# Kernel optimization log

Hardware: AMD Instinct MI355X
Metric: run time of the kernel (lower is better)

Reference implementation:

```python
import jax, jax.numpy as jnp
import numpy as np

N = 50000      # nodes
E = 1_600_000  # edges
IN, H, H2, OUT = 256, 128, 64, 2
EPS = 1e-5     # BatchNorm eps


def setup_inputs() -> dict:
    key = jax.random.key(0)
    ks = jax.random.split(key, 18)
    inp = {
        "x": jax.random.normal(ks[0], (N, IN), dtype=jnp.float32),
        "edge_index": jax.random.randint(ks[1], (2, E), 0, N, dtype=jnp.int64),
        # GCNConv 1
        "W1": jax.random.normal(ks[2], (IN, H), dtype=jnp.float32) / np.sqrt(IN),
        "b1": jnp.zeros((H,), dtype=jnp.float32),
        "g1": jnp.ones((H,), dtype=jnp.float32),
        "be1": jnp.zeros((H,), dtype=jnp.float32),
        "m1": jax.random.normal(ks[3], (H,), dtype=jnp.float32) * 0.1,
        "v1": jax.random.uniform(ks[4], (H,), dtype=jnp.float32, minval=0.5, maxval=1.5),
        # GCNConv 2
        "W2": jax.random.normal(ks[5], (H, H2), dtype=jnp.float32) / np.sqrt(H),
        "b2": jnp.zeros((H2,), dtype=jnp.float32),
        "g2": jnp.ones((H2,), dtype=jnp.float32),
        "be2": jnp.zeros((H2,), dtype=jnp.float32),
        "m2": jax.random.normal(ks[6], (H2,), dtype=jnp.float32) * 0.1,
        "v2": jax.random.uniform(ks[7], (H2,), dtype=jnp.float32, minval=0.5, maxval=1.5),
        # final linear
        "Wl": jax.random.normal(ks[8], (H2, OUT), dtype=jnp.float32) / np.sqrt(H2),
        "bl": jnp.zeros((OUT,), dtype=jnp.float32),
    }
    return inp


def _gcn_conv(x, W, b, src, dst, n_nodes):
    # PyG GCNConv: linear transform, then symmetric-normalized aggregation
    # with self-loops (gcn_norm, improved=False, fill_value=1).
    xw = x @ W                                            # [N, H]
    ones = jnp.ones((src.shape[0],), dtype=x.dtype)
    deg = jax.ops.segment_sum(ones, dst, num_segments=n_nodes) + 1.0  # +1 self-loop
    dinv = jax.lax.rsqrt(deg)                             # deg^{-1/2}
    norm = dinv[src] * dinv[dst]                          # [E]
    msgs = xw[src] * norm[:, None]                        # [E, H] gather
    agg = jax.ops.segment_sum(msgs, dst, num_segments=n_nodes)  # scatter-add
    agg = agg + xw * (1.0 / deg)[:, None]                 # self-loop term
    return agg + b


def _bn_relu(x, gamma, beta, mean, var):
    # inference-mode BatchNorm1d + ReLU
    xhat = (x - mean) * jax.lax.rsqrt(var + EPS)
    return jax.nn.relu(xhat * gamma + beta)


def reference(x, edge_index, W1, b1, g1, be1, m1, v1,
              W2, b2, g2, be2, m2, v2, Wl, bl):
    src, dst = edge_index[0], edge_index[1]
    h = _gcn_conv(x, W1, b1, src, dst, N)
    h = _bn_relu(h, g1, be1, m1, v1)
    # dropout is identity in eval mode
    h = _gcn_conv(h, W2, b2, src, dst, N)
    h = _bn_relu(h, g2, be2, m2, v2)
    return h @ Wl + bl
```

## Files before the change

kernel.cpp:

```cpp
#include <hip/hip_runtime.h>

#define N_NODES 50000
#define N_EDGES 1600000
#define IN_F 256
#define H1_F 128
#define H2_F 64
#define OUT_F 2
#define BN_EPS 1e-5f

#define NBUK 782
#define BCAP 3584
#define CHUNK 8192
#define NCHUNK 196

__device__ __forceinline__ unsigned short f2b(float f) {
    union { float f; unsigned u; } v; v.f = f;
    unsigned r = (v.u + 0x7FFFu + ((v.u >> 16) & 1u)) >> 16;
    return (unsigned short)r;
}
__device__ __forceinline__ float b2f(unsigned short b) {
    union { unsigned u; float f; } v; v.u = ((unsigned)b) << 16;
    return v.f;
}
__device__ __forceinline__ void add2(float& a0, float& a1, unsigned u) {
    union { unsigned u; float f; } lo, hi;
    lo.u = u << 16;
    hi.u = u & 0xFFFF0000u;
    a0 += lo.f; a1 += hi.f;
}

__launch_bounds__(512)
__global__ void chist_kernel(const int* __restrict__ dst, int* __restrict__ h) {
    __shared__ int lh[NBUK];
    const int c = blockIdx.x;
    for (int i = threadIdx.x; i < NBUK; i += 512) lh[i] = 0;
    __syncthreads();
    const int e0 = c * CHUNK;
    const int e1 = min(e0 + CHUNK, N_EDGES);
    for (int e = e0 + threadIdx.x; e < e1; e += 512)
        atomicAdd(&lh[dst[e] >> 6], 1);
    __syncthreads();
    for (int i = threadIdx.x; i < NBUK; i += 512)
        h[c * NBUK + i] = lh[i];
}

__global__ void bscan2_kernel(int* __restrict__ h, int* __restrict__ boff,
                              int* __restrict__ rowptr) {
    __shared__ int tmp[1024];
    const int t = threadIdx.x;
    int tot = 0;
    if (t < NBUK)
        for (int c = 0; c < NCHUNK; ++c) tot += h[c * NBUK + t];
    tmp[t] = tot;
    __syncthreads();
    for (int off = 1; off < 1024; off <<= 1) {
        int a = (t >= off) ? tmp[t - off] : 0;
        __syncthreads();
        tmp[t] += a;
        __syncthreads();
    }
    const int excl = tmp[t] - tot;
    if (t < NBUK) boff[t] = excl;
    if (t == 0) { boff[NBUK] = N_EDGES; rowptr[N_NODES] = N_EDGES; }
    if (t < NBUK) {
        int run = excl;
        for (int c = 0; c < NCHUNK; ++c) {
            int v = h[c * NBUK + t];
            h[c * NBUK + t] = run;
            run += v;
        }
    }
}

__launch_bounds__(512)
__global__ void cscatter_kernel(const int* __restrict__ src, const int* __restrict__ dst,
                                const int* __restrict__ h, unsigned* __restrict__ bedges) {
    __shared__ int cur[NBUK];
    const int c = blockIdx.x;
    for (int i = threadIdx.x; i < NBUK; i += 512) cur[i] = h[c * NBUK + i];
    __syncthreads();
    const int e0 = c * CHUNK;
    const int e1 = min(e0 + CHUNK, N_EDGES);
    for (int e = e0 + threadIdx.x; e < e1; e += 512) {
        int s = src[e];
        int d = dst[e];
        int slot = atomicAdd(&cur[d >> 6], 1);
        bedges[slot] = (unsigned)s | ((unsigned)d << 16);
    }
}

__launch_bounds__(256)
__global__ void build_kernel(const unsigned* __restrict__ bedges, const int* __restrict__ boff,
                             unsigned short* __restrict__ perm, int* __restrict__ rowptr,
                             float* __restrict__ dinv) {
    __shared__ unsigned e_lds[BCAP];
    __shared__ unsigned short p_lds[BCAP];
    __shared__ int ncnt[64], ncur[64];

    const int b = blockIdx.x;
    const int t = threadIdx.x;
    const int start = boff[b];
    const int end   = boff[b + 1];
    const int cnt   = end - start;
    const bool fits = (cnt <= BCAP);

    if (t < 64) ncnt[t] = 0;
    __syncthreads();

    for (int i = t; i < cnt; i += 256) {
        unsigned e = bedges[start + i];
        if (fits) e_lds[i] = e;
        atomicAdd(&ncnt[(e >> 16) & 63], 1);
    }
    __syncthreads();

    if (t == 0) {
        int a = 0;
        for (int i = 0; i < 64; ++i) { ncur[i] = a; a += ncnt[i]; }
    }
    __syncthreads();

    if (t < 64) {
        int node = b * 64 + t;
        if (node < N_NODES) {
            rowptr[node] = start + ncur[t];
            dinv[node]   = rsqrtf((float)ncnt[t] + 1.0f);
        }
    }
    __syncthreads();

    for (int i = t; i < cnt; i += 256) {
        unsigned e = fits ? e_lds[i] : bedges[start + i];
        int slot = atomicAdd(&ncur[(e >> 16) & 63], 1);
        unsigned short s = (unsigned short)(e & 0xFFFFu);
        if (fits) p_lds[slot] = s;
        else      perm[start + slot] = s;
    }
    if (fits) {
        __syncthreads();
        for (int i = t; i < cnt; i += 256) perm[start + i] = p_lds[i];
    }
}

template <typename AT, int BN, int TN>
__launch_bounds__(256)
__global__ void gemm_kernel(const AT* __restrict__ A, const float* __restrict__ B,
                            const float* __restrict__ dscale, unsigned short* __restrict__ C,
                            int M, int K) {
    constexpr int BM = 64;
    constexpr int BK = 16;
    __shared__ float As[BM][BK + 4];
    __shared__ float Bs[BK][BN];

    const int tid  = threadIdx.x;
    const int row0 = blockIdx.x * BM;
    const int tcol = tid & 15;
    const int trow = tid >> 4;

    float acc[4][TN];
#pragma unroll
    for (int i = 0; i < 4; ++i)
#pragma unroll
        for (int j = 0; j < TN; ++j) acc[i][j] = 0.f;

    const int arow = tid >> 2;
    const int acol = (tid & 3) << 2;
    int ar = row0 + arow;
    if (ar >= M) ar = M - 1;

    for (int k0 = 0; k0 < K; k0 += BK) {
        if constexpr (sizeof(AT) == 4) {
            float4 av = *(const float4*)((const float*)A + (size_t)ar * K + k0 + acol);
            *(float4*)(&As[arow][acol]) = av;
        } else {
            ushort4 av = *(const ushort4*)((const unsigned short*)A + (size_t)ar * K + k0 + acol);
            As[arow][acol + 0] = b2f(av.x);
            As[arow][acol + 1] = b2f(av.y);
            As[arow][acol + 2] = b2f(av.z);
            As[arow][acol + 3] = b2f(av.w);
        }
        constexpr int B4 = BN / 4;
#pragma unroll
        for (int l = tid; l < BK * B4; l += 256) {
            int brow = l / B4;
            int bcol = (l % B4) << 2;
            *(float4*)(&Bs[brow][bcol]) =
                *(const float4*)(B + (size_t)(k0 + brow) * BN + bcol);
        }
        __syncthreads();
#pragma unroll
        for (int kk = 0; kk < BK; ++kk) {
            float a[4];
#pragma unroll
            for (int i = 0; i < 4; ++i) a[i] = As[trow * 4 + i][kk];
            float b[TN];
#pragma unroll
            for (int j = 0; j < TN; ++j) b[j] = Bs[kk][tcol * TN + j];
#pragma unroll
            for (int i = 0; i < 4; ++i)
#pragma unroll
                for (int j = 0; j < TN; ++j) acc[i][j] += a[i] * b[j];
        }
        __syncthreads();
    }
#pragma unroll
    for (int i = 0; i < 4; ++i) {
        int r = row0 + trow * 4 + i;
        if (r < M) {
            float ds = dscale[r];
#pragma unroll
            for (int j = 0; j < TN; j += 4) {
                ushort4 o;
                o.x = f2b(acc[i][j + 0] * ds);
                o.y = f2b(acc[i][j + 1] * ds);
                o.z = f2b(acc[i][j + 2] * ds);
                o.w = f2b(acc[i][j + 3] * ds);
                *(ushort4*)(C + (size_t)r * BN + tcol * TN + j) = o;
            }
        }
    }
}

template <int HF, bool FINAL>
__launch_bounds__(256)
__global__ void agg_kernel(const int* __restrict__ rowptr, const unsigned short* __restrict__ perm,
                           const unsigned short* __restrict__ xwb, const float* __restrict__ dinv,
                           const float* __restrict__ bias, const float* __restrict__ g,
                           const float* __restrict__ be, const float* __restrict__ m,
                           const float* __restrict__ v, const float* __restrict__ Wl,
                           const float* __restrict__ bl, void* __restrict__ outp) {
    constexpr int FPQ = HF / 32;
    const int wid = (blockIdx.x * blockDim.x + threadIdx.x) >> 6;
    if (wid >= N_NODES) return;
    const int lane = threadIdx.x & 63;
    const int half = lane >> 5;
    const int l5   = lane & 31;
    const int f0   = l5 * FPQ;
    const int d    = wid;

    float acc[FPQ];
#pragma unroll
    for (int q = 0; q < FPQ; ++q) acc[q] = 0.f;

    if (half == 0) {
        if constexpr (FPQ == 4) {
            uint2 t = *(const uint2*)(xwb + (size_t)d * HF + f0);
            add2(acc[0], acc[1], t.x);
            add2(acc[2], acc[3], t.y);
        } else {
            unsigned t = *(const unsigned*)(xwb + (size_t)d * HF + f0);
            add2(acc[0], acc[1], t);
        }
    }

    const int start = rowptr[d];
    const int end   = rowptr[d + 1];
    for (int base = start; base < end; base += 64) {
        int pidx = base + lane;
        int pv = perm[pidx < end ? pidx : end - 1];
        int ne = end - base;
        if (ne > 64) ne = 64;
        if (ne == 64) {
#pragma unroll
            for (int j = 0; j < 64; j += 2) {
                int s = __shfl(pv, j + half);
                if constexpr (FPQ == 4) {
                    uint2 t = *(const uint2*)(xwb + (size_t)s * HF + f0);
                    add2(acc[0], acc[1], t.x);
                    add2(acc[2], acc[3], t.y);
                } else {
                    unsigned t = *(const unsigned*)(xwb + (size_t)s * HF + f0);
                    add2(acc[0], acc[1], t);
                }
            }
        } else {
            for (int j = 0; j < ne; j += 2) {
                int s = __shfl(pv, j + half);
                if (j + half < ne) {
                    if constexpr (FPQ == 4) {
                        uint2 t = *(const uint2*)(xwb + (size_t)s * HF + f0);
                        add2(acc[0], acc[1], t.x);
                        add2(acc[2], acc[3], t.y);
                    } else {
                        unsigned t = *(const unsigned*)(xwb + (size_t)s * HF + f0);
                        add2(acc[0], acc[1], t);
                    }
                }
            }
        }
    }

#pragma unroll
    for (int q = 0; q < FPQ; ++q) acc[q] += __shfl_xor(acc[q], 32);

    const float dv = dinv[d];
    float y[FPQ];
#pragma unroll
    for (int q = 0; q < FPQ; ++q) {
        int f = f0 + q;
        float s  = g[f] * rsqrtf(v[f] + BN_EPS);
        float sh = (bias[f] - m[f]) * s + be[f];
        y[q] = fmaxf(acc[q] * dv * s + sh, 0.f);
    }

    if constexpr (!FINAL) {
        if (half == 0) {
            if constexpr (FPQ == 4) {
                ushort4 o;
                o.x = f2b(y[0]); o.y = f2b(y[1]); o.z = f2b(y[2]); o.w = f2b(y[3]);
                *(ushort4*)((unsigned short*)outp + (size_t)d * HF + f0) = o;
            }
        }
    } else {
        float p0 = y[0] * Wl[f0 * 2 + 0] + y[1] * Wl[(f0 + 1) * 2 + 0];
        float p1 = y[0] * Wl[f0 * 2 + 1] + y[1] * Wl[(f0 + 1) * 2 + 1];
#pragma unroll
        for (int off = 16; off > 0; off >>= 1) {
            p0 += __shfl_xor(p0, off);
            p1 += __shfl_xor(p1, off);
        }
        if (lane == 0) {
            float* o = (float*)outp;
            o[(size_t)d * 2 + 0] = p0 + bl[0];
            o[(size_t)d * 2 + 1] = p1 + bl[1];
        }
    }
}

extern "C" void kernel_launch(void* const* d_in, const int* in_sizes, int n_in,
                              void* d_out, int out_size, void* d_ws, size_t ws_size,
                              hipStream_t stream) {
    const float* x   = (const float*)d_in[0];
    const int*   ei  = (const int*)d_in[1];
    const float* W1  = (const float*)d_in[2];
    const float* b1  = (const float*)d_in[3];
    const float* g1  = (const float*)d_in[4];
    const float* be1 = (const float*)d_in[5];
    const float* m1  = (const float*)d_in[6];
    const float* v1  = (const float*)d_in[7];
    const float* W2  = (const float*)d_in[8];
    const float* b2  = (const float*)d_in[9];
    const float* g2  = (const float*)d_in[10];
    const float* be2 = (const float*)d_in[11];
    const float* m2  = (const float*)d_in[12];
    const float* v2  = (const float*)d_in[13];
    const float* Wl  = (const float*)d_in[14];
    const float* bl  = (const float*)d_in[15];

    const int* src = ei;
    const int* dst = ei + N_EDGES;

    int*            h      = (int*)d_ws;
    int*            boff   = h + NCHUNK * NBUK;
    int*            rowptr = boff + 1024;
    float*          dinv   = (float*)(rowptr + 50016);
    unsigned*       bedges = (unsigned*)(dinv + 50016);
    unsigned short* perm   = (unsigned short*)(bedges + N_EDGES);
    unsigned short* xwb    = perm + N_EDGES;
    unsigned short* h1b    = xwb + (size_t)N_NODES * H1_F;

    chist_kernel<<<NCHUNK, 512, 0, stream>>>(dst, h);
    bscan2_kernel<<<1, 1024, 0, stream>>>(h, boff, rowptr);
    cscatter_kernel<<<NCHUNK, 512, 0, stream>>>(src, dst, h, bedges);
    build_kernel<<<NBUK, 256, 0, stream>>>(bedges, boff, perm, rowptr, dinv);

    gemm_kernel<float, H1_F, 8><<<(N_NODES + 63) / 64, 256, 0, stream>>>(
        x, W1, dinv, xwb, N_NODES, IN_F);
    agg_kernel<H1_F, false><<<(N_NODES * 64) / 256, 256, 0, stream>>>(
        rowptr, perm, xwb, dinv, b1, g1, be1, m1, v1, nullptr, nullptr, h1b);

    gemm_kernel<unsigned short, H2_F, 4><<<(N_NODES + 63) / 64, 256, 0, stream>>>(
        h1b, W2, dinv, xwb, N_NODES, H1_F);
    agg_kernel<H2_F, true><<<(N_NODES * 64) / 256, 256, 0, stream>>>(
        rowptr, perm, xwb, dinv, b2, g2, be2, m2, v2, Wl, bl, (float*)d_out);
}
```

Baseline: 267.3 us.

## Replace FP32 tiled GEMMs with bf16 MFMA matrix-core GEMMs

After: 254.4 us. -4.8%, faster.

```diff
diff --git a/kernel.cpp b/kernel.cpp
--- a/kernel.cpp
+++ b/kernel.cpp
@@ -12,6 +12,9 @@
 #define BCAP 3584
 #define CHUNK 8192
 #define NCHUNK 196
+
+typedef __attribute__((ext_vector_type(8))) short bf16x8;
+typedef __attribute__((ext_vector_type(4))) float f32x4;
 
 __device__ __forceinline__ unsigned short f2b(float f) {
     union { float f; unsigned u; } v; v.f = f;
@@ -142,81 +145,65 @@
     }
 }
 
-template <typename AT, int BN, int TN>
+__global__ void wt_kernel(const float* __restrict__ W, unsigned short* __restrict__ WT,
+                          int K, int N) {
+    int i = blockIdx.x * blockDim.x + threadIdx.x;
+    if (i < N * K) {
+        int n = i / K, k = i % K;
+        WT[i] = f2b(W[(size_t)k * N + n]);
+    }
+}
+
+template <int KSTEPS, int NTILES, bool A_BF16>
 __launch_bounds__(256)
-__global__ void gemm_kernel(const AT* __restrict__ A, const float* __restrict__ B,
-                            const float* __restrict__ dscale, unsigned short* __restrict__ C,
-                            int M, int K) {
-    constexpr int BM = 64;
-    constexpr int BK = 16;
-    __shared__ float As[BM][BK + 4];
-    __shared__ float Bs[BK][BN];
-
-    const int tid  = threadIdx.x;
-    const int row0 = blockIdx.x * BM;
-    const int tcol = tid & 15;
-    const int trow = tid >> 4;
-
-    float acc[4][TN];
-#pragma unroll
-    for (int i = 0; i < 4; ++i)
-#pragma unroll
-        for (int j = 0; j < TN; ++j) acc[i][j] = 0.f;
-
-    const int arow = tid >> 2;
-    const int acol = (tid & 3) << 2;
-    int ar = row0 + arow;
-    if (ar >= M) ar = M - 1;
-
-    for (int k0 = 0; k0 < K; k0 += BK) {
-        if constexpr (sizeof(AT) == 4) {
-            float4 av = *(const float4*)((const float*)A + (size_t)ar * K + k0 + acol);
-            *(float4*)(&As[arow][acol]) = av;
+__global__ void mfma_gemm_kernel(const void* __restrict__ Ap, const unsigned short* __restrict__ BT,
+                                 const float* __restrict__ dscale, unsigned short* __restrict__ C,
+                                 int M) {
+    constexpr int K  = KSTEPS * 32;
+    constexpr int NF = NTILES * 16;
+    const int wave = threadIdx.x >> 6;
+    const int lane = threadIdx.x & 63;
+    const int r0   = (blockIdx.x * 4 + wave) * 16;
+    const int m    = lane & 15;
+    const int kb   = lane >> 4;
+
+    int arow = r0 + m;
+    if (arow >= M) arow = M - 1;
+
+    f32x4 acc[NTILES];
+#pragma unroll
+    for (int nt = 0; nt < NTILES; ++nt) acc[nt] = (f32x4)(0.f);
+
+#pragma unroll
+    for (int ks = 0; ks < KSTEPS; ++ks) {
+        const int k0 = ks * 32 + kb * 8;
+        bf16x8 a;
+        if constexpr (A_BF16) {
+            a = *(const bf16x8*)((const unsigned short*)Ap + (size_t)arow * K + k0);
         } else {
-            ushort4 av = *(const ushort4*)((const unsigned short*)A + (size_t)ar * K + k0 + acol);
-            As[arow][acol + 0] = b2f(av.x);
-            As[arow][acol + 1] = b2f(av.y);
-            As[arow][acol + 2] = b2f(av.z);
-            As[arow][acol + 3] = b2f(av.w);
-        }
-        constexpr int B4 = BN / 4;
-#pragma unroll
-        for (int l = tid; l < BK * B4; l += 256) {
-            int brow = l / B4;
-            int bcol = (l % B4) << 2;
-            *(float4*)(&Bs[brow][bcol]) =
-                *(const float4*)(B + (size_t)(k0 + brow) * BN + bcol);
-        }
-        __syncthreads();
-#pragma unroll
-        for (int kk = 0; kk < BK; ++kk) {
-            float a[4];
-#pragma unroll
-            for (int i = 0; i < 4; ++i) a[i] = As[trow * 4 + i][kk];
-            float b[TN];
-#pragma unroll
-            for (int j = 0; j < TN; ++j) b[j] = Bs[kk][tcol * TN + j];
-#pragma unroll
-            for (int i = 0; i < 4; ++i)
-#pragma unroll
-                for (int j = 0; j < TN; ++j) acc[i][j] += a[i] * b[j];
-        }
-        __syncthreads();
-    }
-#pragma unroll
-    for (int i = 0; i < 4; ++i) {
-        int r = row0 + trow * 4 + i;
+            const float* af = (const float*)Ap + (size_t)arow * K + k0;
+            float4 lo = *(const float4*)af;
+            float4 hi = *(const float4*)(af + 4);
+            union { bf16x8 v; unsigned short u[8]; } pk;
+            pk.u[0] = f2b(lo.x); pk.u[1] = f2b(lo.y); pk.u[2] = f2b(lo.z); pk.u[3] = f2b(lo.w);
+            pk.u[4] = f2b(hi.x); pk.u[5] = f2b(hi.y); pk.u[6] = f2b(hi.z); pk.u[7] = f2b(hi.w);
+            a = pk.v;
+        }
+#pragma unroll
+        for (int nt = 0; nt < NTILES; ++nt) {
+            bf16x8 b = *(const bf16x8*)(BT + (size_t)(nt * 16 + m) * K + k0);
+            acc[nt] = __builtin_amdgcn_mfma_f32_16x16x32_bf16(a, b, acc[nt], 0, 0, 0);
+        }
+    }
+
+#pragma unroll
+    for (int reg = 0; reg < 4; ++reg) {
+        const int r = r0 + kb * 4 + reg;
         if (r < M) {
-            float ds = dscale[r];
-#pragma unroll
-            for (int j = 0; j < TN; j += 4) {
-                ushort4 o;
-                o.x = f2b(acc[i][j + 0] * ds);
-                o.y = f2b(acc[i][j + 1] * ds);
-                o.z = f2b(acc[i][j + 2] * ds);
-                o.w = f2b(acc[i][j + 3] * ds);
-                *(ushort4*)(C + (size_t)r * BN + tcol * TN + j) = o;
-            }
+            const float ds = dscale[r];
+#pragma unroll
+            for (int nt = 0; nt < NTILES; ++nt)
+                C[(size_t)r * NF + nt * 16 + m] = f2b(acc[nt][reg] * ds);
         }
     }
 }
@@ -358,19 +345,24 @@
     unsigned short* perm   = (unsigned short*)(bedges + N_EDGES);
     unsigned short* xwb    = perm + N_EDGES;
     unsigned short* h1b    = xwb + (size_t)N_NODES * H1_F;
+    unsigned short* w1t    = h1b + (size_t)N_NODES * H1_F;
+    unsigned short* w2t    = w1t + H1_F * IN_F;
 
     chist_kernel<<<NCHUNK, 512, 0, stream>>>(dst, h);
     bscan2_kernel<<<1, 1024, 0, stream>>>(h, boff, rowptr);
     cscatter_kernel<<<NCHUNK, 512, 0, stream>>>(src, dst, h, bedges);
     build_kernel<<<NBUK, 256, 0, stream>>>(bedges, boff, perm, rowptr, dinv);
 
-    gemm_kernel<float, H1_F, 8><<<(N_NODES + 63) / 64, 256, 0, stream>>>(
-        x, W1, dinv, xwb, N_NODES, IN_F);
+    wt_kernel<<<(H1_F * IN_F + 255) / 256, 256, 0, stream>>>(W1, w1t, IN_F, H1_F);
+    wt_kernel<<<(H2_F * H1_F + 255) / 256, 256, 0, stream>>>(W2, w2t, H1_F, H2_F);
+
+    mfma_gemm_kernel<IN_F / 32, H1_F / 16, false><<<(N_NODES + 63) / 64, 256, 0, stream>>>(
+        x, w1t, dinv, xwb, N_NODES);
     agg_kernel<H1_F, false><<<(N_NODES * 64) / 256, 256, 0, stream>>>(
         rowptr, perm, xwb, dinv, b1, g1, be1, m1, v1, nullptr, nullptr, h1b);
 
-    gemm_kernel<unsigned short, H2_F, 4><<<(N_NODES + 63) / 64, 256, 0, stream>>>(
-        h1b, W2, dinv, xwb, N_NODES, H1_F);
+    mfma_gemm_kernel<H1_F / 32, H2_F / 16, true><<<(N_NODES + 63) / 64, 256, 0, stream>>>(
+        h1b, w2t, dinv, xwb, N_NODES);
     agg_kernel<H2_F, true><<<(N_NODES * 64) / 256, 256, 0, stream>>>(
         rowptr, perm, xwb, dinv, b2, g2, be2, m2, v2, Wl, bl, (float*)d_out);
 }
```
